# Optimization experiments

Hardware: AMD Instinct MI355X
Metric: run time of the kernel (lower is better)

The kernel has to match this reference:

```python
import jax, jax.numpy as jnp
import numpy as np

NUM_ANCHORS = 9  # 3 ratios * 3 sizes


def setup_inputs() -> dict:
    key = jax.random.key(0)
    k0, k1, k2, k3 = jax.random.split(key, 4)
    B, C, H, W = 4, 256, 200, 336
    resnet_features = jax.random.normal(k0, (B, C, H, W), dtype=jnp.float32)
    # 3x3 conv: C -> 512
    W1 = jax.random.normal(k1, (512, C, 3, 3), dtype=jnp.float32) * 0.02
    b1 = jnp.zeros((512,), dtype=jnp.float32)
    # 1x1 cls head: 512 -> 9*2
    Wc = jax.random.normal(k2, (NUM_ANCHORS * 2, 512), dtype=jnp.float32) * 0.02
    bc = jnp.zeros((NUM_ANCHORS * 2,), dtype=jnp.float32)
    # 1x1 bbox head: 512 -> 9*4
    Wb = jax.random.normal(k3, (NUM_ANCHORS * 4, 512), dtype=jnp.float32) * 0.02
    bb = jnp.zeros((NUM_ANCHORS * 4,), dtype=jnp.float32)
    return {"resnet_features": resnet_features, "W1": W1, "b1": b1,
            "Wc": Wc, "bc": bc, "Wb": Wb, "bb": bb}


def reference(resnet_features, W1, b1, Wc, bc, Wb, bb):
    B = resnet_features.shape[0]
    # conv3x3 + ReLU (padding=1 -> SAME)
    feat = jax.lax.conv_general_dilated(
        resnet_features, W1, window_strides=(1, 1), padding='SAME',
        dimension_numbers=('NCHW', 'OIHW', 'NCHW'))
    feat = jax.nn.relu(feat + b1[None, :, None, None])  # [B,512,H,W]
    # 1x1 conv heads as channel contractions
    cls = jnp.einsum('bchw,oc->bohw', feat, Wc) + bc[None, :, None, None]
    box = jnp.einsum('bchw,oc->bohw', feat, Wb) + bb[None, :, None, None]
    # permute(0,2,3,1).view(B,-1,2/4)
    anchor_cls_score = jnp.transpose(cls, (0, 2, 3, 1)).reshape(B, -1, 2)
    anchor_bboxdelta = jnp.transpose(box, (0, 2, 3, 1)).reshape(B, -1, 4)
    return anchor_cls_score, anchor_bboxdelta
```

## Files before the change

kernel.cpp:

```cpp
#include <hip/hip_runtime.h>
#include <hip/hip_bf16.h>
#include <stdint.h>

#define B_   4
#define C_   256
#define H_   200
#define W_   336
#define OC_  512
#define HP_  202
#define WP_  338
#define M_   (B_*H_*W_)
#define MTILES (M_/128)
#define OUT0_ (M_*18)
#define OUT_TOTAL_ (M_*54)

#define XP_ELEMS  ((size_t)B_*HP_*WP_*C_)
#define XP_BYTES  (XP_ELEMS*2)
#define W1T_ELEMS ((size_t)9*OC_*C_)
#define W1T_OFF   XP_BYTES
#define WHB_OFF   (W1T_OFF + W1T_ELEMS*2)

typedef unsigned short ushortT;
typedef __attribute__((ext_vector_type(8))) short bf16x8;
typedef __attribute__((ext_vector_type(4))) float f32x4;

static __device__ __forceinline__ ushortT f2bf(float x) {
    union { float f; uint32_t u; } v; v.f = x;
    uint32_t r = v.u + 0x7fff + ((v.u >> 16) & 1);
    return (ushortT)(r >> 16);
}

__global__ __launch_bounds__(256) void zero_halo(ushortT* __restrict__ Xp) {
    int i = blockIdx.x * 256 + threadIdx.x;
    if (i >= 4 * 1076 * 32) return;
    int pix = i >> 5, ch = (i & 31) * 8;
    int b = pix / 1076, r = pix % 1076;
    int h, w;
    if (r < 338)      { h = 0;   w = r; }
    else if (r < 676) { h = 201; w = r - 338; }
    else { r -= 676; h = 1 + (r >> 1); w = (r & 1) ? 337 : 0; }
    size_t dst = (((size_t)b*HP_ + h)*WP_ + w)*C_ + ch;
    *(uint4*)(Xp + dst) = make_uint4(0, 0, 0, 0);
}

__global__ __launch_bounds__(256) void pad_transpose(const float* __restrict__ X,
                                                     ushortT* __restrict__ Xp) {
    int bid = blockIdx.x;
    int wc = bid % 6; int bh = bid / 6;
    int h = bh % H_;  int b = bh / H_;
    int w0 = wc * 64;
    int t = threadIdx.x;
    __shared__ ushortT tile[64 * 65];

    for (int c0 = 0; c0 < C_; c0 += 64) {
        if (c0) __syncthreads();
        int col  = t & 63;
        int rowb = t >> 6;
        #pragma unroll
        for (int rr = 0; rr < 16; ++rr) {
            int row = rowb * 16 + rr;
            int w = w0 + col;
            float val = 0.f;
            if (w < W_)
                val = X[(((size_t)(b*C_ + c0 + row))*H_ + h)*W_ + w];
            tile[row*65 + col] = f2bf(val);
        }
        __syncthreads();
        int pixel = t >> 2;
        int csub  = (t & 3) * 16;
        int w = w0 + pixel;
        if (w < W_) {
            union { ushortT u[16]; uint4 q[2]; } vals;
            #pragma unroll
            for (int j = 0; j < 16; ++j)
                vals.u[j] = tile[(csub + j)*65 + pixel];
            size_t dst = (((size_t)b*HP_ + (h+1))*WP_ + (w+1))*C_ + c0 + csub;
            *(uint4*)(Xp + dst)     = vals.q[0];
            *(uint4*)(Xp + dst + 8) = vals.q[1];
        }
    }
}

__global__ __launch_bounds__(256) void prep_w1(const float* __restrict__ W1,
                                               ushortT* __restrict__ W1t) {
    int t = blockIdx.x * 256 + threadIdx.x;
    if (t >= OC_*C_) return;
    const float* src = W1 + (size_t)t * 9;
    #pragma unroll
    for (int rs = 0; rs < 9; ++rs)
        W1t[(size_t)rs*OC_*C_ + t] = f2bf(src[rs]);
}

__global__ __launch_bounds__(256) void prep_whb(const float* __restrict__ Wc,
                                                const float* __restrict__ Wb,
                                                ushortT* __restrict__ Whb) {
    int t = blockIdx.x * 256 + threadIdx.x;
    if (t >= 64*512) return;
    int o = t >> 9, oc = t & 511;
    float v = 0.f;
    if (o < 18) v = Wc[o*512 + oc];
    else if (o < 54) v = Wb[(o-18)*512 + oc];
    Whb[t] = f2bf(v);
}

#define CONV_GRID 2100

__global__ __launch_bounds__(512, 2) void conv_rpn(
    const ushortT* __restrict__ Xp, const ushortT* __restrict__ W1t,
    const float* __restrict__ b1,  const ushortT* __restrict__ Whb,
    const float* __restrict__ bc,  const float* __restrict__ bb,
    float* __restrict__ out)
{
    extern __shared__ ushortT smem[];

    const int tid  = threadIdx.x;
    const int wave = tid >> 6;
    const int lane = tid & 63;
    const int col  = lane & 15;
    const int quad = lane >> 4;
    const int c7   = col & 7;
    const int wm   = (wave >> 2) * 64;
    const int wn   = (wave & 3) * 128;

    const int bid = blockIdx.x;
    const int xcd = bid & 7, ib = bid >> 3;
    const int mtile = (xcd < 4) ? (xcd*263 + ib) : (1052 + (xcd-4)*262 + ib);

    const int r8     = lane >> 3;
    const int lchunk = ((lane & 7) ^ r8) * 8;

    size_t pixA[2];
    #pragma unroll
    for (int i = 0; i < 2; ++i) {
        int m = mtile*128 + wave*16 + i*8 + r8;
        int b = m / (H_*W_);
        int rem = m % (H_*W_);
        int hh = rem / W_;
        int ww = rem % W_;
        pixA[i] = (((size_t)b*HP_ + hh)*WP_ + ww)*C_ + lchunk;
    }
    const size_t bbase = ((size_t)(wave*64 + r8))*C_ + lchunk;

    f32x4 acc[4][8] = {};

    auto STAGE = [&](int t, int buf) {
        const int rs = t >> 2;
        const int cs = (t & 3) << 6;
        const int roff = ((rs/3)*WP_ + (rs%3)) * C_;
        const size_t wsrc = (size_t)rs*OC_*C_ + bbase + cs;
        ushortT* Ab = smem + buf*8192  + (wave*16)*64;
        ushortT* Bb = smem + 16384 + buf*32768 + (wave*64)*64;
        #pragma unroll
        for (int i = 0; i < 2; ++i)
            __builtin_amdgcn_global_load_lds(
                (const __attribute__((address_space(1))) uint32_t*)(Xp + pixA[i] + roff + cs),
                (__attribute__((address_space(3))) uint32_t*)(Ab + i*8*64), 16, 0, 0);
        #pragma unroll
        for (int i = 0; i < 8; ++i)
            __builtin_amdgcn_global_load_lds(
                (const __attribute__((address_space(1))) uint32_t*)(W1t + wsrc + (size_t)i*8*C_),
                (__attribute__((address_space(3))) uint32_t*)(Bb + i*8*64), 16, 0, 0);
    };

    STAGE(0, 0);

    #pragma unroll 1
    for (int t = 0; t < 36; ++t) {
        const int cur = t & 1;
        if (t < 35) {
            STAGE(t + 1, cur ^ 1);
            asm volatile("s_waitcnt vmcnt(10)" ::: "memory");
        } else {
            asm volatile("s_waitcnt vmcnt(0)" ::: "memory");
        }
        __builtin_amdgcn_sched_barrier(0);
        __builtin_amdgcn_s_barrier();
        __builtin_amdgcn_sched_barrier(0);

        const ushortT* Al = smem + cur*8192;
        const ushortT* Bl = smem + 16384 + cur*32768;
        #pragma unroll
        for (int kk = 0; kk < 2; ++kk) {
            const int pc = ((kk*4 + quad) ^ c7) * 8;
            bf16x8 af[4], bfr[8];
            #pragma unroll
            for (int mt = 0; mt < 4; ++mt)
                af[mt] = *(const bf16x8*)&Al[(wm + mt*16 + col)*64 + pc];
            #pragma unroll
            for (int nt = 0; nt < 8; ++nt)
                bfr[nt] = *(const bf16x8*)&Bl[(wn + nt*16 + col)*64 + pc];
            __builtin_amdgcn_s_setprio(1);
            #pragma unroll
            for (int mt = 0; mt < 4; ++mt)
                #pragma unroll
                for (int nt = 0; nt < 8; ++nt)
                    acc[mt][nt] = __builtin_amdgcn_mfma_f32_16x16x32_bf16(
                        af[mt], bfr[nt], acc[mt][nt], 0, 0, 0);
            __builtin_amdgcn_s_setprio(0);
        }
        asm volatile("s_waitcnt lgkmcnt(0)" ::: "memory");
        __builtin_amdgcn_sched_barrier(0);
        __builtin_amdgcn_s_barrier();
        __builtin_amdgcn_sched_barrier(0);
    }

    ushortT* Fsm = smem;
    float b1v[8];
    #pragma unroll
    for (int nt = 0; nt < 8; ++nt) b1v[nt] = b1[wn + nt*16 + col];
    #pragma unroll
    for (int mt = 0; mt < 4; ++mt)
        #pragma unroll
        for (int nt = 0; nt < 8; ++nt) {
            const float bv = b1v[nt];
            #pragma unroll
            for (int rg = 0; rg < 4; ++rg) {
                int row  = wm + mt*16 + quad*4 + rg;
                int colc = wn + nt*16 + col;
                float v = fmaxf(acc[mt][nt][rg] + bv, 0.f);
                int pos = (((colc >> 3) ^ (row & 7)) << 3) | (colc & 7);
                Fsm[row*512 + pos] = f2bf(v);
            }
        }
    __syncthreads();

    f32x4 hacc[4] = {};
    const int hrow = wave*16 + col;
    const int h7   = col & 7;
    const ushortT* Fr = Fsm + hrow*512;
    #pragma unroll
    for (int ks = 0; ks < 16; ++ks) {
        bf16x8 ah = *(const bf16x8*)&Fr[((ks*4 + quad) ^ h7) << 3];
        #pragma unroll
        for (int nt = 0; nt < 4; ++nt) {
            bf16x8 bh = *(const bf16x8*)&Whb[(nt*16 + col)*512 + ks*32 + quad*8];
            hacc[nt] = __builtin_amdgcn_mfma_f32_16x16x32_bf16(
                ah, bh, hacc[nt], 0, 0, 0);
        }
    }

    #pragma unroll
    for (int nt = 0; nt < 4; ++nt) {
        int o = nt*16 + col;
        float bias = (o < 18) ? bc[o] : (o < 54 ? bb[o - 18] : 0.f);
        #pragma unroll
        for (int rg = 0; rg < 4; ++rg) {
            size_t p = (size_t)mtile*128 + wave*16 + quad*4 + rg;
            float v = hacc[nt][rg] + bias;
            if (o < 18)      out[p*18 + o] = v;
            else if (o < 54) out[OUT0_ + p*36 + (o - 18)] = v;
        }
    }
}

extern "C" void kernel_launch(void* const* d_in, const int* in_sizes, int n_in,
                              void* d_out, int out_size, void* d_ws, size_t ws_size,
                              hipStream_t stream) {
    const float* X  = (const float*)d_in[0];
    const float* W1 = (const float*)d_in[1];
    const float* b1 = (const float*)d_in[2];
    const float* Wc = (const float*)d_in[3];
    const float* bc = (const float*)d_in[4];
    const float* Wb = (const float*)d_in[5];
    const float* bb = (const float*)d_in[6];
    float* out = (float*)d_out;

    ushortT* Xp  = (ushortT*)d_ws;
    ushortT* W1t = (ushortT*)((char*)d_ws + W1T_OFF);
    ushortT* Whb = (ushortT*)((char*)d_ws + WHB_OFF);

    static bool attr_set = false;
    if (!attr_set) {
        hipFuncSetAttribute((const void*)conv_rpn,
                            hipFuncAttributeMaxDynamicSharedMemorySize, 163840);
        attr_set = true;
    }

    zero_halo<<<(4*1076*32 + 255)/256, 256, 0, stream>>>(Xp);
    pad_transpose<<<B_*H_*6, 256, 0, stream>>>(X, Xp);
    prep_w1<<<(OC_*C_ + 255)/256, 256, 0, stream>>>(W1, W1t);
    prep_whb<<<(64*512 + 255)/256, 256, 0, stream>>>(Wc, Wb, Whb);
    conv_rpn<<<CONV_GRID, 512, 163840, stream>>>(Xp, W1t, b1, Whb, bc, bb, out);
}
```

Before: 1.150 ms.

## Interleave global-to-LDS prefetch chunks with MFMA sub-phases in conv main loop

Splits each K-step of the implicit-GEMM conv into four sub-phases (two k-halves times two N-halves). The next tile's global-to-LDS loads are issued in four chunks spread across those sub-phases instead of one burst, and the vmcnt wait drops to only the first chunk. The goal is to overlap memory issue with MFMA work more evenly and cut per-phase fragment register use. The cost is more workgroup barriers per iteration and tighter ordering assumptions between LDS reads and the async writes into the other buffer.

```diff
diff --git a/kernel.cpp b/kernel.cpp
--- a/kernel.cpp
+++ b/kernel.cpp
@@ -105,6 +105,10 @@
 
 #define CONV_GRID 2100
 
+#define GLD(gsrc, ldst) __builtin_amdgcn_global_load_lds( \
+    (const __attribute__((address_space(1))) uint32_t*)(gsrc), \
+    (__attribute__((address_space(3))) uint32_t*)(ldst), 16, 0, 0)
+
 __global__ __launch_bounds__(512, 2) void conv_rpn(
     const ushortT* __restrict__ Xp, const ushortT* __restrict__ W1t,
     const float* __restrict__ b1,  const ushortT* __restrict__ Whb,
@@ -143,65 +147,93 @@
 
     f32x4 acc[4][8] = {};
 
-    auto STAGE = [&](int t, int buf) {
-        const int rs = t >> 2;
-        const int cs = (t & 3) << 6;
-        const int roff = ((rs/3)*WP_ + (rs%3)) * C_;
-        const size_t wsrc = (size_t)rs*OC_*C_ + bbase + cs;
+    auto STAGE_CHUNK = [&](int q, int buf, size_t aoff, size_t woff) {
         ushortT* Ab = smem + buf*8192  + (wave*16)*64;
         ushortT* Bb = smem + 16384 + buf*32768 + (wave*64)*64;
-        #pragma unroll
-        for (int i = 0; i < 2; ++i)
-            __builtin_amdgcn_global_load_lds(
-                (const __attribute__((address_space(1))) uint32_t*)(Xp + pixA[i] + roff + cs),
-                (__attribute__((address_space(3))) uint32_t*)(Ab + i*8*64), 16, 0, 0);
-        #pragma unroll
-        for (int i = 0; i < 8; ++i)
-            __builtin_amdgcn_global_load_lds(
-                (const __attribute__((address_space(1))) uint32_t*)(W1t + wsrc + (size_t)i*8*C_),
-                (__attribute__((address_space(3))) uint32_t*)(Bb + i*8*64), 16, 0, 0);
+        switch (q) {
+        case 0:
+            GLD(Xp + pixA[0] + aoff, Ab);
+            GLD(Xp + pixA[1] + aoff, Ab + 8*64);
+            GLD(W1t + woff,          Bb);
+            break;
+        case 1:
+            GLD(W1t + woff + (size_t)1*8*C_, Bb + 1*8*64);
+            GLD(W1t + woff + (size_t)2*8*C_, Bb + 2*8*64);
+            GLD(W1t + woff + (size_t)3*8*C_, Bb + 3*8*64);
+            break;
+        case 2:
+            GLD(W1t + woff + (size_t)4*8*C_, Bb + 4*8*64);
+            GLD(W1t + woff + (size_t)5*8*C_, Bb + 5*8*64);
+            break;
+        default:
+            GLD(W1t + woff + (size_t)6*8*C_, Bb + 6*8*64);
+            GLD(W1t + woff + (size_t)7*8*C_, Bb + 7*8*64);
+        }
     };
 
-    STAGE(0, 0);
+    STAGE_CHUNK(0, 0, 0, bbase);
+    STAGE_CHUNK(1, 0, 0, bbase);
+    STAGE_CHUNK(2, 0, 0, bbase);
+    STAGE_CHUNK(3, 0, 0, bbase);
 
     #pragma unroll 1
     for (int t = 0; t < 36; ++t) {
         const int cur = t & 1;
-        if (t < 35) {
-            STAGE(t + 1, cur ^ 1);
-            asm volatile("s_waitcnt vmcnt(10)" ::: "memory");
-        } else {
-            asm volatile("s_waitcnt vmcnt(0)" ::: "memory");
-        }
-        __builtin_amdgcn_sched_barrier(0);
-        __builtin_amdgcn_s_barrier();
-        __builtin_amdgcn_sched_barrier(0);
-
         const ushortT* Al = smem + cur*8192;
         const ushortT* Bl = smem + 16384 + cur*32768;
-        #pragma unroll
-        for (int kk = 0; kk < 2; ++kk) {
+        const bool pf = (t < 35);
+        size_t aoffn = 0, woffn = 0;
+        if (pf) {
+            int tn = t + 1;
+            int rsn = tn >> 2, csn = (tn & 3) << 6;
+            aoffn = (size_t)((rsn/3)*WP_ + (rsn%3))*C_ + csn;
+            woffn = (size_t)rsn*OC_*C_ + bbase + csn;
+        }
+
+        #pragma unroll
+        for (int q = 0; q < 4; ++q) {
+            const int kk = q >> 1, nh = q & 1;
             const int pc = ((kk*4 + quad) ^ c7) * 8;
-            bf16x8 af[4], bfr[8];
-            #pragma unroll
-            for (int mt = 0; mt < 4; ++mt)
-                af[mt] = *(const bf16x8*)&Al[(wm + mt*16 + col)*64 + pc];
-            #pragma unroll
-            for (int nt = 0; nt < 8; ++nt)
-                bfr[nt] = *(const bf16x8*)&Bl[(wn + nt*16 + col)*64 + pc];
+            bf16x8 af[4], bfr[4];
+            if (q == 0) {
+                if (pf) {
+                    STAGE_CHUNK(0, cur ^ 1, aoffn, woffn);
+                    asm volatile("s_waitcnt vmcnt(3)" ::: "memory");
+                } else {
+                    asm volatile("s_waitcnt vmcnt(0)" ::: "memory");
+                }
+                __builtin_amdgcn_sched_barrier(0);
+                __builtin_amdgcn_s_barrier();
+                __builtin_amdgcn_sched_barrier(0);
+                #pragma unroll
+                for (int mt = 0; mt < 4; ++mt)
+                    af[mt] = *(const bf16x8*)&Al[(wm + mt*16 + col)*64 + pc];
+                #pragma unroll
+                for (int nt = 0; nt < 4; ++nt)
+                    bfr[nt] = *(const bf16x8*)&Bl[(wn + nh*64 + nt*16 + col)*64 + pc];
+            } else {
+                #pragma unroll
+                for (int mt = 0; mt < 4; ++mt)
+                    af[mt] = *(const bf16x8*)&Al[(wm + mt*16 + col)*64 + pc];
+                #pragma unroll
+                for (int nt = 0; nt < 4; ++nt)
+                    bfr[nt] = *(const bf16x8*)&Bl[(wn + nh*64 + nt*16 + col)*64 + pc];
+                if (pf) STAGE_CHUNK(q, cur ^ 1, aoffn, woffn);
+                __builtin_amdgcn_s_barrier();
+            }
+            asm volatile("s_waitcnt lgkmcnt(0)" ::: "memory");
+            __builtin_amdgcn_sched_barrier(0);
             __builtin_amdgcn_s_setprio(1);
             #pragma unroll
             for (int mt = 0; mt < 4; ++mt)
                 #pragma unroll
-                for (int nt = 0; nt < 8; ++nt)
-                    acc[mt][nt] = __builtin_amdgcn_mfma_f32_16x16x32_bf16(
-                        af[mt], bfr[nt], acc[mt][nt], 0, 0, 0);
+                for (int nt = 0; nt < 4; ++nt)
+                    acc[mt][nh*4 + nt] = __builtin_amdgcn_mfma_f32_16x16x32_bf16(
+                        af[mt], bfr[nt], acc[mt][nh*4 + nt], 0, 0, 0);
             __builtin_amdgcn_s_setprio(0);
-        }
-        asm volatile("s_waitcnt lgkmcnt(0)" ::: "memory");
-        __builtin_amdgcn_sched_barrier(0);
-        __builtin_amdgcn_s_barrier();
-        __builtin_amdgcn_sched_barrier(0);
+            __builtin_amdgcn_sched_barrier(0);
+            __builtin_amdgcn_s_barrier();
+        }
     }
 
     ushortT* Fsm = smem;
```

Measured after the change: 1.172 ms. About the same (+1.9%).
